# Optimization experiments

Measured on AMD Instinct MI355X. Metric: run time of the kernel, lower is better.

The kernel has to match this reference:

```python
import jax, jax.numpy as jnp
import numpy as np

NG = 128          # grid points per axis
FEAT = 16         # feature size
WIDTH = 64        # mlp hidden width
OUT = 1
NPTS = 262144
NUM_POS = 3       # sinusoidal frequencies
IN_MLP = FEAT + NUM_POS * 3


def setup_inputs() -> dict:
    key = jax.random.key(0)
    k1, k2, k3, k4, k5, k6 = jax.random.split(key, 6)
    x = jax.random.uniform(k1, (NPTS, 3), dtype=jnp.float32)
    grid = jax.random.normal(k2, (NG, NG, NG, FEAT), dtype=jnp.float32)
    lim1 = 1.0 / np.sqrt(IN_MLP)
    lim2 = 1.0 / np.sqrt(WIDTH)
    w1 = jax.random.uniform(k3, (WIDTH, IN_MLP), minval=-lim1, maxval=lim1, dtype=jnp.float32)
    b1 = jax.random.uniform(k4, (WIDTH,), minval=-lim1, maxval=lim1, dtype=jnp.float32)
    w2 = jax.random.uniform(k5, (OUT, WIDTH), minval=-lim2, maxval=lim2, dtype=jnp.float32)
    b2 = jax.random.uniform(k6, (OUT,), minval=-lim2, maxval=lim2, dtype=jnp.float32)
    return {"x": x, "grid": grid, "w1": w1, "b1": b1, "w2": w2, "b2": b2}


def _cubic_weights(t):
    # Catmull-Rom (a=-0.5) cubic convolution weights over 4-point stencil.
    # t: (..., ) fractional coordinate in [0,1). returns (..., 4)
    t2 = t * t
    t3 = t2 * t
    w0 = 0.5 * (-t3 + 2.0 * t2 - t)
    w1 = 0.5 * (3.0 * t3 - 5.0 * t2 + 2.0)
    w2 = 0.5 * (-3.0 * t3 + 4.0 * t2 + t)
    w3 = 0.5 * (t3 - t2)
    return jnp.stack([w0, w1, w2, w3], axis=-1)


def _forward(x, grid, w1, b1, w2, b2):
    n = grid.shape[0]
    # domain [0,1]^3, uniform spacing h = 1/(n-1); block_frac == fractional cell coord
    u = x * (n - 1.0)                       # (N,3) grid-space coords
    i0 = jnp.floor(u).astype(jnp.int32)
    t = u - i0                              # (N,3) in [0,1)
    offs = jnp.arange(-1, 3, dtype=jnp.int32)
    idx = jnp.clip(i0[:, :, None] + offs, 0, n - 1)   # (N,3,4)
    w = _cubic_weights(t)                   # (N,3,4)
    # 4x4x4 gather per point: (N,4,4,4,F)
    g = grid[idx[:, 0, :, None, None], idx[:, 1, None, :, None], idx[:, 2, None, None, :]]
    feat = jnp.einsum('na,nb,nc,nabcf->nf', w[:, 0], w[:, 1], w[:, 2], g)  # (N,F)
    # sinusoidal pos-encoding: sin(2*pi*k * frac), k=1..3, layout (k, dim) flattened
    mult = 2.0 * jnp.pi * jnp.arange(1, NUM_POS + 1, dtype=x.dtype)        # (3,)
    pos = jnp.sin(mult[None, :, None] * t[:, None, :]).reshape(x.shape[0], -1)  # (N,9)
    h = jnp.concatenate([feat, pos], axis=-1)           # (N, F+9)
    hid = jax.nn.swish(h @ w1.T + b1)                   # (N, WIDTH)
    return hid @ w2.T + b2                              # (N, OUT)


def reference(x, grid, w1, b1, w2, b2):
    return _forward(x, grid, w1, b1, w2, b2)
```

## Files before the change

kernel.cpp:

```cpp
#include <hip/hip_runtime.h>
#include <cmath>

#define NGRID 128
#define FEAT 16
#define WIDTH 64
#define NPTS 262144
#define IN_MLP 25
#define NBUCKETS 4096

#define WS_PERM_OFF (NBUCKETS * 4)
#define WS_KEY_OFF  (NBUCKETS * 4 + NPTS * 4)
#define WS_NEEDED   (NBUCKETS * 4 + NPTS * 8)

__device__ __forceinline__ int bucket_of(const float* __restrict__ x, int p) {
    int key = 0;
    #pragma unroll
    for (int d = 0; d < 3; ++d) {
        int i0 = (int)floorf(x[3 * p + d] * 127.0f);
        i0 = i0 < 0 ? 0 : (i0 > 126 ? 126 : i0);
        key = (key << 4) | (i0 >> 3);
    }
    return key;
}

__global__ void zero_hist_kernel(int* __restrict__ hist) {
    hist[blockIdx.x * 256 + threadIdx.x] = 0;
}

__global__ void hist_kernel(const float* __restrict__ x, int* __restrict__ hist,
                            int* __restrict__ keys) {
    const int p = blockIdx.x * blockDim.x + threadIdx.x;
    if (p >= NPTS) return;
    const int k = bucket_of(x, p);
    keys[p] = k;
    atomicAdd(&hist[k], 1);
}

__global__ __launch_bounds__(1024) void scan_kernel(int* __restrict__ hist) {
    __shared__ int lds[1024];
    const int t = threadIdx.x;
    int4 v = ((int4*)hist)[t];
    lds[t] = v.x + v.y + v.z + v.w;
    __syncthreads();
    #pragma unroll
    for (int off = 1; off < 1024; off <<= 1) {
        int val = lds[t];
        int add = (t >= off) ? lds[t - off] : 0;
        __syncthreads();
        lds[t] = val + add;
        __syncthreads();
    }
    const int excl = (t == 0) ? 0 : lds[t - 1];
    int4 o;
    o.x = excl;
    o.y = excl + v.x;
    o.z = excl + v.x + v.y;
    o.w = excl + v.x + v.y + v.z;
    ((int4*)hist)[t] = o;
}

__global__ void scatter_kernel(const int* __restrict__ keys, int* __restrict__ offs,
                               int* __restrict__ perm) {
    const int p = blockIdx.x * blockDim.x + threadIdx.x;
    if (p >= NPTS) return;
    const int pos = atomicAdd(&offs[keys[p]], 1);
    perm[pos] = p;
}

__device__ __forceinline__ void fma4(float4& a, float w, const float4 c) {
    a.x = fmaf(w, c.x, a.x);
    a.y = fmaf(w, c.y, a.y);
    a.z = fmaf(w, c.z, a.z);
    a.w = fmaf(w, c.w, a.w);
}

template <bool SORTED>
__global__ __launch_bounds__(128, 4) void gridnet_kernel(
    const float* __restrict__ x,
    const float* __restrict__ grid,
    const float* __restrict__ w1,
    const float* __restrict__ b1,
    const float* __restrict__ w2,
    const float* __restrict__ b2,
    const int* __restrict__ perm,
    float* __restrict__ out)
{
    const int bid = blockIdx.x;
    const int swz = SORTED ? ((bid & 7) * 256 + (bid >> 3)) : bid;
    const int gid = swz * 128 + threadIdx.x;
    const int p = SORTED ? perm[gid] : gid;

    int   offa[4], offb[4], offc[4];
    float wx[4], wy[4], wz[4];
    float t[3];
    #pragma unroll
    for (int d = 0; d < 3; ++d) {
        const float u  = x[3 * p + d] * 127.0f;
        const float fu = floorf(u);
        const float td = u - fu;
        t[d] = td;
        const int i0 = (int)fu;
        const float t2 = td * td;
        const float t3 = t2 * td;
        float w0 = 0.5f * (-t3 + 2.0f * t2 - td);
        float w1v = 0.5f * (3.0f * t3 - 5.0f * t2 + 2.0f);
        float w2v = 0.5f * (-3.0f * t3 + 4.0f * t2 + td);
        float w3 = 0.5f * (t3 - t2);
        #pragma unroll
        for (int o = 0; o < 4; ++o) {
            int v = i0 - 1 + o;
            v = v < 0 ? 0 : (v > 127 ? 127 : v);
            if (d == 0) offa[o] = v * 65536;
            if (d == 1) offb[o] = v * 512;
            if (d == 2) offc[o] = v * 4;
        }
        float* wp = (d == 0) ? wx : (d == 1) ? wy : wz;
        wp[0] = w0; wp[1] = w1v; wp[2] = w2v; wp[3] = w3;
    }

    float4 acc0 = make_float4(0.f, 0.f, 0.f, 0.f);
    float4 acc1 = acc0, acc2 = acc0, acc3 = acc0;
    const float4* __restrict__ g4 = (const float4*)grid;

    #pragma unroll 1
    for (int a = 0; a < 4; ++a) {
        const float wa = wx[a];
        #pragma unroll 2
        for (int b = 0; b < 4; ++b) {
            const float wab = wa * wy[b];
            const int   rb  = offa[a] + offb[b];
            #pragma unroll
            for (int c = 0; c < 4; ++c) {
                const float w = wab * wz[c];
                const float4* cell = g4 + (rb + offc[c]);
                fma4(acc0, w, cell[0]);
                fma4(acc1, w, cell[1]);
                fma4(acc2, w, cell[2]);
                fma4(acc3, w, cell[3]);
            }
        }
    }

    float h[IN_MLP];
    h[0]  = acc0.x; h[1]  = acc0.y; h[2]  = acc0.z; h[3]  = acc0.w;
    h[4]  = acc1.x; h[5]  = acc1.y; h[6]  = acc1.z; h[7]  = acc1.w;
    h[8]  = acc2.x; h[9]  = acc2.y; h[10] = acc2.z; h[11] = acc2.w;
    h[12] = acc3.x; h[13] = acc3.y; h[14] = acc3.z; h[15] = acc3.w;

    #pragma unroll
    for (int k = 0; k < 3; ++k) {
        #pragma unroll
        for (int d = 0; d < 3; ++d) {
            h[16 + k * 3 + d] = __builtin_amdgcn_sinf((float)(k + 1) * t[d]);
        }
    }

    float o = b2[0];
    #pragma unroll 4
    for (int j = 0; j < WIDTH; ++j) {
        float hj = b1[j];
        #pragma unroll
        for (int k = 0; k < IN_MLP; ++k) {
            hj = fmaf(h[k], w1[j * IN_MLP + k], hj);
        }
        const float sig = 1.0f / (1.0f + __expf(-hj));
        o = fmaf(hj * sig, w2[j], o);
    }
    out[p] = o;
}

extern "C" void kernel_launch(void* const* d_in, const int* in_sizes, int n_in,
                              void* d_out, int out_size, void* d_ws, size_t ws_size,
                              hipStream_t stream) {
    const float* x    = (const float*)d_in[0];
    const float* grid = (const float*)d_in[1];
    const float* w1   = (const float*)d_in[2];
    const float* b1   = (const float*)d_in[3];
    const float* w2   = (const float*)d_in[4];
    const float* b2   = (const float*)d_in[5];
    float* out = (float*)d_out;

    if (ws_size >= (size_t)WS_NEEDED) {
        int* hist = (int*)d_ws;
        int* perm = (int*)((char*)d_ws + WS_PERM_OFF);
        int* keys = (int*)((char*)d_ws + WS_KEY_OFF);
        zero_hist_kernel<<<NBUCKETS / 256, 256, 0, stream>>>(hist);
        hist_kernel<<<NPTS / 256, 256, 0, stream>>>(x, hist, keys);
        scan_kernel<<<1, 1024, 0, stream>>>(hist);
        scatter_kernel<<<NPTS / 256, 256, 0, stream>>>(keys, hist, perm);
        gridnet_kernel<true><<<NPTS / 128, 128, 0, stream>>>(
            x, grid, w1, b1, w2, b2, perm, out);
    } else {
        gridnet_kernel<false><<<NPTS / 128, 128, 0, stream>>>(
            x, grid, w1, b1, w2, b2, nullptr, out);
    }
}
```

Baseline: 589.3 us.

## Split each point's gather across two lanes and scatter sorted coordinates directly

```diff
diff --git a/kernel.cpp b/kernel.cpp
--- a/kernel.cpp
+++ b/kernel.cpp
@@ -8,30 +8,27 @@
 #define IN_MLP 25
 #define NBUCKETS 4096
 
-#define WS_PERM_OFF (NBUCKETS * 4)
-#define WS_KEY_OFF  (NBUCKETS * 4 + NPTS * 4)
-#define WS_NEEDED   (NBUCKETS * 4 + NPTS * 8)
-
-__device__ __forceinline__ int bucket_of(const float* __restrict__ x, int p) {
+#define WS_KEY_OFF (NBUCKETS * 4)
+#define WS_XS_OFF  (NBUCKETS * 4 + NPTS * 4)
+#define WS_NEEDED  (NBUCKETS * 4 + NPTS * 4 + NPTS * 16)
+
+__device__ __forceinline__ int bucket_of3(float x0, float x1, float x2) {
     int key = 0;
+    const float c[3] = {x0, x1, x2};
     #pragma unroll
     for (int d = 0; d < 3; ++d) {
-        int i0 = (int)floorf(x[3 * p + d] * 127.0f);
+        int i0 = (int)floorf(c[d] * 127.0f);
         i0 = i0 < 0 ? 0 : (i0 > 126 ? 126 : i0);
         key = (key << 4) | (i0 >> 3);
     }
     return key;
-}
-
-__global__ void zero_hist_kernel(int* __restrict__ hist) {
-    hist[blockIdx.x * 256 + threadIdx.x] = 0;
 }
 
 __global__ void hist_kernel(const float* __restrict__ x, int* __restrict__ hist,
                             int* __restrict__ keys) {
     const int p = blockIdx.x * blockDim.x + threadIdx.x;
     if (p >= NPTS) return;
-    const int k = bucket_of(x, p);
+    const int k = bucket_of3(x[3 * p], x[3 * p + 1], x[3 * p + 2]);
     keys[p] = k;
     atomicAdd(&hist[k], 1);
 }
@@ -59,12 +56,15 @@
     ((int4*)hist)[t] = o;
 }
 
-__global__ void scatter_kernel(const int* __restrict__ keys, int* __restrict__ offs,
-                               int* __restrict__ perm) {
+__global__ void scatter_kernel(const float* __restrict__ x,
+                               const int* __restrict__ keys,
+                               int* __restrict__ offs,
+                               float4* __restrict__ xs) {
     const int p = blockIdx.x * blockDim.x + threadIdx.x;
     if (p >= NPTS) return;
     const int pos = atomicAdd(&offs[keys[p]], 1);
-    perm[pos] = p;
+    xs[pos] = make_float4(x[3 * p], x[3 * p + 1], x[3 * p + 2],
+                          __int_as_float(p));
 }
 
 __device__ __forceinline__ void fma4(float4& a, float w, const float4 c) {
@@ -75,27 +75,39 @@
 }
 
 template <bool SORTED>
-__global__ __launch_bounds__(128, 4) void gridnet_kernel(
+__global__ __launch_bounds__(256, 8) void gridnet_kernel(
     const float* __restrict__ x,
     const float* __restrict__ grid,
     const float* __restrict__ w1,
     const float* __restrict__ b1,
     const float* __restrict__ w2,
     const float* __restrict__ b2,
-    const int* __restrict__ perm,
+    const float4* __restrict__ xs,
     float* __restrict__ out)
 {
     const int bid = blockIdx.x;
     const int swz = SORTED ? ((bid & 7) * 256 + (bid >> 3)) : bid;
-    const int gid = swz * 128 + threadIdx.x;
-    const int p = SORTED ? perm[gid] : gid;
+    const int g   = swz * 256 + threadIdx.x;
+    const int s    = g >> 1;
+    const int half = g & 1;
+
+    float xc[3];
+    int p;
+    if (SORTED) {
+        const float4 v = xs[s];
+        xc[0] = v.x; xc[1] = v.y; xc[2] = v.z;
+        p = __float_as_int(v.w);
+    } else {
+        p = s;
+        xc[0] = x[3 * p]; xc[1] = x[3 * p + 1]; xc[2] = x[3 * p + 2];
+    }
 
     int   offa[4], offb[4], offc[4];
     float wx[4], wy[4], wz[4];
     float t[3];
     #pragma unroll
     for (int d = 0; d < 3; ++d) {
-        const float u  = x[3 * p + d] * 127.0f;
+        const float u  = xc[d] * 127.0f;
         const float fu = floorf(u);
         const float td = u - fu;
         t[d] = td;
@@ -123,12 +135,14 @@
     const float4* __restrict__ g4 = (const float4*)grid;
 
     #pragma unroll 1
-    for (int a = 0; a < 4; ++a) {
+    for (int aj = 0; aj < 2; ++aj) {
+        const int   a  = 2 * half + aj;
         const float wa = wx[a];
-        #pragma unroll 2
+        const int   oa = offa[a];
+        #pragma unroll 1
         for (int b = 0; b < 4; ++b) {
             const float wab = wa * wy[b];
-            const int   rb  = offa[a] + offb[b];
+            const int   rb  = oa + offb[b];
             #pragma unroll
             for (int c = 0; c < 4; ++c) {
                 const float w = wab * wz[c];
@@ -142,10 +156,12 @@
     }
 
     float h[IN_MLP];
-    h[0]  = acc0.x; h[1]  = acc0.y; h[2]  = acc0.z; h[3]  = acc0.w;
-    h[4]  = acc1.x; h[5]  = acc1.y; h[6]  = acc1.z; h[7]  = acc1.w;
-    h[8]  = acc2.x; h[9]  = acc2.y; h[10] = acc2.z; h[11] = acc2.w;
-    h[12] = acc3.x; h[13] = acc3.y; h[14] = acc3.z; h[15] = acc3.w;
+    h[0]=acc0.x; h[1]=acc0.y; h[2]=acc0.z;  h[3]=acc0.w;
+    h[4]=acc1.x; h[5]=acc1.y; h[6]=acc1.z;  h[7]=acc1.w;
+    h[8]=acc2.x; h[9]=acc2.y; h[10]=acc2.z; h[11]=acc2.w;
+    h[12]=acc3.x;h[13]=acc3.y;h[14]=acc3.z; h[15]=acc3.w;
+    #pragma unroll
+    for (int i = 0; i < 16; ++i) h[i] += __shfl_xor(h[i], 1);
 
     #pragma unroll
     for (int k = 0; k < 3; ++k) {
@@ -166,7 +182,7 @@
         const float sig = 1.0f / (1.0f + __expf(-hj));
         o = fmaf(hj * sig, w2[j], o);
     }
-    out[p] = o;
+    if (half == 0) out[p] = o;
 }
 
 extern "C" void kernel_launch(void* const* d_in, const int* in_sizes, int n_in,
@@ -180,18 +196,21 @@
     const float* b2   = (const float*)d_in[5];
     float* out = (float*)d_out;
 
+    const int nthreads = 2 * NPTS;
+    const int nblocks  = nthreads / 256;
+
     if (ws_size >= (size_t)WS_NEEDED) {
-        int* hist = (int*)d_ws;
-        int* perm = (int*)((char*)d_ws + WS_PERM_OFF);
-        int* keys = (int*)((char*)d_ws + WS_KEY_OFF);
-        zero_hist_kernel<<<NBUCKETS / 256, 256, 0, stream>>>(hist);
-        hist_kernel<<<NPTS / 256, 256, 0, stream>>>(x, hist, keys);
+        int*    hist = (int*)d_ws;
+        int*    keys = (int*)((char*)d_ws + WS_KEY_OFF);
+        float4* xs   = (float4*)((char*)d_ws + WS_XS_OFF);
+        hipMemsetAsync(hist, 0, NBUCKETS * 4, stream);
+        hist_kernel<<<NPTS / 512, 512, 0, stream>>>(x, hist, keys);
         scan_kernel<<<1, 1024, 0, stream>>>(hist);
-        scatter_kernel<<<NPTS / 256, 256, 0, stream>>>(keys, hist, perm);
-        gridnet_kernel<true><<<NPTS / 128, 128, 0, stream>>>(
-            x, grid, w1, b1, w2, b2, perm, out);
+        scatter_kernel<<<NPTS / 512, 512, 0, stream>>>(x, keys, hist, xs);
+        gridnet_kernel<true><<<nblocks, 256, 0, stream>>>(
+            x, grid, w1, b1, w2, b2, xs, out);
     } else {
-        gridnet_kernel<false><<<NPTS / 128, 128, 0, stream>>>(
+        gridnet_kernel<false><<<nblocks, 256, 0, stream>>>(
             x, grid, w1, b1, w2, b2, nullptr, out);
     }
 }
```

Result: faster. 574.1 us (-2.6%).
